# Kernel tuning notes

Measured on AMD Instinct MI355X. Metric: run time of the kernel, lower is better.

## Reference

```python
import jax, jax.numpy as jnp
import numpy as np

B, C, N, K, D = 4, 64, 40960, 16, 128
EPS = 1e-5  # BatchNorm2d default eps


def _bn_relu(x, g, b, m, v):
    # inference BN over channel axis 1, then ReLU (pt_utils.Conv2d default activation)
    scale = g / jnp.sqrt(v + EPS)
    shift = b - m * scale
    return jax.nn.relu(x * scale[None, :, None, None] + shift[None, :, None, None])


def setup_inputs() -> dict:
    key = jax.random.key(0)
    ks = jax.random.split(key, 16)
    feature = jax.random.normal(ks[0], (B, C, N, 1), jnp.float32)
    neigh_idx = jax.random.randint(ks[1], (B, N, K), 0, N)
    w1 = jax.random.normal(ks[2], (C, C), jnp.float32) * 0.05
    w2 = jax.random.normal(ks[3], (D, C), jnp.float32) * 0.05
    w3 = jax.random.normal(ks[4], (D, C), jnp.float32) * 0.05
    def bn(kg, km, kv, n):
        g = 1.0 + 0.1 * jax.random.normal(kg, (n,), jnp.float32)
        b = 0.1 * jax.random.normal(km, (n,), jnp.float32)
        m = 0.1 * jax.random.normal(kv, (n,), jnp.float32)
        v = jax.random.uniform(jax.random.fold_in(kv, 1), (n,), jnp.float32, 0.5, 1.5)
        return g, b, m, v
    g1, b1, m1, v1 = bn(ks[5], ks[6], ks[7], C)
    g2, b2, m2, v2 = bn(ks[8], ks[9], ks[10], D)
    g3, b3, m3, v3 = bn(ks[11], ks[12], ks[13], D)
    return dict(feature=feature, neigh_idx=neigh_idx,
                w1=w1, g1=g1, b1=b1, m1=m1, v1=v1,
                w2=w2, g2=g2, b2=b2, m2=m2, v2=v2,
                w3=w3, g3=g3, b3=b3, m3=m3, v3=v3)


def reference(feature, neigh_idx, w1, g1, b1, m1, v1, w2, g2, b2, m2, v2,
              w3, g3, b3, m3, v3):
    # gather_neighbour: feature [B,C,N,1], neigh_idx [B,N,K] -> [B,C,N,K]
    f = feature[:, :, :, 0]                                   # [B,C,N]
    f_neigh = jax.vmap(lambda fb, ib: fb[:, ib])(f, neigh_idx)  # [B,C,N,K]
    # mlp1: 1x1 conv + BN + ReLU
    h = jnp.einsum('oc,bcnk->bonk', w1, f_neigh)
    h = _bn_relu(h, g1, b1, m1, v1)
    # sum over neighbors
    h = jnp.sum(h, axis=-1, keepdims=True)                    # [B,C,N,1]
    # mlp2
    h = jnp.einsum('oc,bcnk->bonk', w2, h)
    h = _bn_relu(h, g2, b2, m2, v2)
    # mlp3 on original feature (residual branch)
    s = jnp.einsum('oc,bcnk->bonk', w3, feature)
    s = _bn_relu(s, g3, b3, m3, v3)
    return h + s                                              # [B,D,N,1]
```

## Files before the change

kernel.cpp:

```cpp
#include <hip/hip_runtime.h>

#define EPSV 1e-5f
constexpr int Bb = 4, Cc = 64, Nn = 40960, Kk = 16, Dd = 128;
constexpr int G = 5;
constexpr int TPB = Nn / 16;

typedef float f32x4 __attribute__((ext_vector_type(4)));
typedef __bf16 bf16x8 __attribute__((ext_vector_type(8)));
typedef unsigned short us8 __attribute__((ext_vector_type(8)));
typedef unsigned short us4 __attribute__((ext_vector_type(4)));

__device__ inline unsigned short f2bf(float x) {
    unsigned u = __builtin_bit_cast(unsigned, x);
    u += 0x7FFFu + ((u >> 16) & 1u);
    return (unsigned short)(u >> 16);
}

__global__ __launch_bounds__(256) void prep_weights(
    const float* __restrict__ w1, const float* __restrict__ g1, const float* __restrict__ b1,
    const float* __restrict__ m1, const float* __restrict__ v1,
    const float* __restrict__ w2, const float* __restrict__ g2, const float* __restrict__ b2,
    const float* __restrict__ m2, const float* __restrict__ v2,
    const float* __restrict__ w3, const float* __restrict__ g3, const float* __restrict__ b3,
    const float* __restrict__ m3, const float* __restrict__ v3,
    unsigned short* __restrict__ w1s, unsigned short* __restrict__ w2s, unsigned short* __restrict__ w3s,
    float* __restrict__ sh1, float* __restrict__ sh2, float* __restrict__ sh3) {
    const int e = blockIdx.x * 256 + threadIdx.x;
    if (e < 4096) {
        const int o = e >> 6;
        const float sc = g1[o] * rsqrtf(v1[o] + EPSV);
        w1s[e] = f2bf(w1[e] * sc);
    } else if (e < 12288) {
        const int i = e - 4096, o = i >> 6;
        const float sc = g2[o] * rsqrtf(v2[o] + EPSV);
        w2s[i] = f2bf(w2[i] * sc);
    } else if (e < 20480) {
        const int i = e - 12288, o = i >> 6;
        const float sc = g3[o] * rsqrtf(v3[o] + EPSV);
        w3s[i] = f2bf(w3[i] * sc);
    }
    if (e < 64) sh1[e] = b1[e] - m1[e] * (g1[e] * rsqrtf(v1[e] + EPSV));
    else if (e < 192) { const int d = e - 64;  sh2[d] = b2[d] - m2[d] * (g2[d] * rsqrtf(v2[d] + EPSV)); }
    else if (e < 320) { const int d = e - 192; sh3[d] = b3[d] - m3[d] * (g3[d] * rsqrtf(v3[d] + EPSV)); }
}

__global__ __launch_bounds__(256) void passA(const float* __restrict__ f,
                                             const unsigned short* __restrict__ w1s,
                                             unsigned short* __restrict__ G1) {
    __shared__ float s[64 * 65];
    __shared__ __attribute__((aligned(16))) unsigned short sg1[64 * 72];

    const int tid = threadIdx.x, w = tid >> 6, lane = tid & 63;
    const int c15 = lane & 15, q = lane >> 4;
    const int b = blockIdx.x / 640;
    const int n0 = (blockIdx.x % 640) * 64;

    const float* src = f + ((size_t)b * Cc + w * 16) * Nn + n0 + lane;
#pragma unroll
    for (int i = 0; i < 16; ++i) s[(w * 16 + i) * 65 + lane] = src[(size_t)i * Nn];

    const int o1 = w * 16 + c15;
    bf16x8 bw1[2];
#pragma unroll
    for (int ks = 0; ks < 2; ++ks)
        bw1[ks] = __builtin_bit_cast(bf16x8, *(const uint4*)(w1s + o1 * 64 + ks * 32 + q * 8));
    __syncthreads();

#pragma unroll
    for (int mt = 0; mt < 4; ++mt) {
        const int pt = mt * 16 + c15;
        us8 A0, A1;
#pragma unroll
        for (int j = 0; j < 8; ++j) A0[j] = f2bf(s[(q * 8 + j) * 65 + pt]);
#pragma unroll
        for (int j = 0; j < 8; ++j) A1[j] = f2bf(s[(32 + q * 8 + j) * 65 + pt]);
        f32x4 g = {0.f, 0.f, 0.f, 0.f};
        g = __builtin_amdgcn_mfma_f32_16x16x32_bf16(__builtin_bit_cast(bf16x8, A0), bw1[0], g, 0, 0, 0);
        g = __builtin_amdgcn_mfma_f32_16x16x32_bf16(__builtin_bit_cast(bf16x8, A1), bw1[1], g, 0, 0, 0);
#pragma unroll
        for (int r = 0; r < 4; ++r) sg1[(mt * 16 + q * 4 + r) * 72 + o1] = f2bf(g[r]);
    }
    __syncthreads();

    {
        const int p = tid >> 2, ck = tid & 3;
        const uint4 v0 = *(const uint4*)(sg1 + p * 72 + ck * 16);
        const uint4 v1 = *(const uint4*)(sg1 + p * 72 + ck * 16 + 8);
        unsigned short* dst = G1 + ((size_t)b * Nn + n0 + p) * 64 + ck * 16;
        *(uint4*)dst = v0;
        *(uint4*)(dst + 8) = v1;
    }
}

__global__ __launch_bounds__(256, 4) void passB(
    const unsigned short* __restrict__ G1, const float* __restrict__ f,
    const int* __restrict__ idx,
    const unsigned short* __restrict__ w2s, const unsigned short* __restrict__ w3s,
    const float* __restrict__ sh1, const float* __restrict__ sh2, const float* __restrict__ sh3,
    float* __restrict__ out) {
    __shared__ __attribute__((aligned(16))) unsigned short s_h1[16 * 72];
    __shared__ float s_out[16 * 132];

    const int tid  = threadIdx.x;
    const int wave = tid >> 6;
    const int lane = tid & 63;
    const int c15  = lane & 15;
    const int q    = lane >> 4;
    const int pg   = tid >> 4;
    const int cg   = tid & 15;

    const int t0  = blockIdx.x * G;
    const int b   = t0 / TPB;
    const int nb0 = (t0 - b * TPB) * 16;

    float sh2v[2], sh3v[2];
    bf16x8 bw2[2][2], bw3[2][2];
#pragma unroll
    for (int nt = 0; nt < 2; ++nt) {
        const int d = wave * 32 + nt * 16 + c15;
        sh2v[nt] = sh2[d];
        sh3v[nt] = sh3[d];
#pragma unroll
        for (int ks = 0; ks < 2; ++ks) {
            bw2[nt][ks] = __builtin_bit_cast(bf16x8, *(const uint4*)(w2s + d * 64 + ks * 32 + q * 8));
            bw3[nt][ks] = __builtin_bit_cast(bf16x8, *(const uint4*)(w3s + d * 64 + ks * 32 + q * 8));
        }
    }
    float shA[4];
#pragma unroll
    for (int j = 0; j < 4; ++j) shA[j] = sh1[cg * 4 + j];

    const unsigned short* G1b = G1 + (size_t)b * Nn * 64;
    const float* fb0 = f + (size_t)b * Cc * Nn;

    for (int g = 0; g < G; ++g) {
        const int n0 = nb0 + g * 16;

        const float* fown = fb0 + n0 + c15;
        us8 F0, F1;
#pragma unroll
        for (int j = 0; j < 8; ++j) F0[j] = f2bf(fown[(size_t)(q * 8 + j) * Nn]);
#pragma unroll
        for (int j = 0; j < 8; ++j) F1[j] = f2bf(fown[(size_t)(32 + q * 8 + j) * Nn]);

        const int myidx = idx[((size_t)b * Nn + n0) * Kk + tid];

        float a0 = 0.f, a1 = 0.f, a2 = 0.f, a3 = 0.f;
#pragma unroll
        for (int k = 0; k < 16; ++k) {
            const int nb = __shfl(myidx, (pg & 3) * 16 + k, 64);
            const uint2 d2 = *(const uint2*)(G1b + (size_t)nb * 64 + cg * 4);
            const float f0 = __builtin_bit_cast(float, d2.x << 16);
            const float f1 = __builtin_bit_cast(float, d2.x & 0xffff0000u);
            const float f2v = __builtin_bit_cast(float, d2.y << 16);
            const float f3 = __builtin_bit_cast(float, d2.y & 0xffff0000u);
            a0 += fmaxf(f0 + shA[0], 0.f);
            a1 += fmaxf(f1 + shA[1], 0.f);
            a2 += fmaxf(f2v + shA[2], 0.f);
            a3 += fmaxf(f3 + shA[3], 0.f);
        }

        __syncthreads();
        us4 hv;
        hv[0] = f2bf(a0); hv[1] = f2bf(a1); hv[2] = f2bf(a2); hv[3] = f2bf(a3);
        *(us4*)(s_h1 + pg * 72 + cg * 4) = hv;
        __syncthreads();

        const unsigned short* h1row = s_h1 + c15 * 72;
        const bf16x8 ah0 = __builtin_bit_cast(bf16x8, *(const uint4*)(h1row + q * 8));
        const bf16x8 ah1 = __builtin_bit_cast(bf16x8, *(const uint4*)(h1row + 32 + q * 8));
        const bf16x8 af0 = __builtin_bit_cast(bf16x8, F0);
        const bf16x8 af1 = __builtin_bit_cast(bf16x8, F1);

#pragma unroll
        for (int nt = 0; nt < 2; ++nt) {
            f32x4 h2 = {sh2v[nt], sh2v[nt], sh2v[nt], sh2v[nt]};
            f32x4 s3 = {sh3v[nt], sh3v[nt], sh3v[nt], sh3v[nt]};
            h2 = __builtin_amdgcn_mfma_f32_16x16x32_bf16(ah0, bw2[nt][0], h2, 0, 0, 0);
            h2 = __builtin_amdgcn_mfma_f32_16x16x32_bf16(ah1, bw2[nt][1], h2, 0, 0, 0);
            s3 = __builtin_amdgcn_mfma_f32_16x16x32_bf16(af0, bw3[nt][0], s3, 0, 0, 0);
            s3 = __builtin_amdgcn_mfma_f32_16x16x32_bf16(af1, bw3[nt][1], s3, 0, 0, 0);
            const int d = wave * 32 + nt * 16 + c15;
#pragma unroll
            for (int r = 0; r < 4; ++r) {
                const int p = q * 4 + r;
                s_out[p * 132 + d] = fmaxf(h2[r], 0.f) + fmaxf(s3[r], 0.f);
            }
        }
        __syncthreads();

        {
            const int d = tid >> 1, half = tid & 1;
            float v[8];
#pragma unroll
            for (int i = 0; i < 8; ++i) v[i] = s_out[(half * 8 + i) * 132 + d];
            float* dst = out + ((size_t)b * Dd + d) * Nn + n0 + half * 8;
            __builtin_nontemporal_store((f32x4){v[0], v[1], v[2], v[3]}, (f32x4*)dst);
            __builtin_nontemporal_store((f32x4){v[4], v[5], v[6], v[7]}, (f32x4*)(dst + 4));
        }
    }
}

extern "C" void kernel_launch(void* const* d_in, const int* in_sizes, int n_in,
                              void* d_out, int out_size, void* d_ws, size_t ws_size,
                              hipStream_t stream) {
    const float* feature = (const float*)d_in[0];
    const int*   neigh   = (const int*)d_in[1];
    const float* w1 = (const float*)d_in[2];
    const float* g1 = (const float*)d_in[3];
    const float* b1 = (const float*)d_in[4];
    const float* m1 = (const float*)d_in[5];
    const float* v1 = (const float*)d_in[6];
    const float* w2 = (const float*)d_in[7];
    const float* g2 = (const float*)d_in[8];
    const float* b2 = (const float*)d_in[9];
    const float* m2 = (const float*)d_in[10];
    const float* v2 = (const float*)d_in[11];
    const float* w3 = (const float*)d_in[12];
    const float* g3 = (const float*)d_in[13];
    const float* b3 = (const float*)d_in[14];
    const float* m3 = (const float*)d_in[15];
    const float* v3 = (const float*)d_in[16];
    float* out = (float*)d_out;

    char* ws = (char*)d_ws;
    unsigned short* G1  = (unsigned short*)ws;
    unsigned short* w1s = (unsigned short*)(ws + 20971520);
    unsigned short* w2s = (unsigned short*)(ws + 20971520 + 8192);
    unsigned short* w3s = (unsigned short*)(ws + 20971520 + 24576);
    float* sh1 = (float*)(ws + 20971520 + 40960);
    float* sh2 = (float*)(ws + 20971520 + 41216);
    float* sh3 = (float*)(ws + 20971520 + 41728);

    prep_weights<<<80, 256, 0, stream>>>(w1, g1, b1, m1, v1, w2, g2, b2, m2, v2,
                                         w3, g3, b3, m3, v3, w1s, w2s, w3s, sh1, sh2, sh3);
    passA<<<Bb * 640, 256, 0, stream>>>(feature, w1s, G1);
    passB<<<(Bb * TPB) / G, 256, 0, stream>>>(G1, feature, neigh, w2s, w3s,
                                              sh1, sh2, sh3, out);
}
```

Measured before the change: 227.8 us.

## Stage transposed bf16 features in passA and store outputs directly from MFMA

passA now also writes a point-major bf16 copy of the input features, provided the workspace is large enough, so passB loads its residual-branch operand as contiguous 16-byte vectors instead of 16 strided fp32 loads per lane. passB drops the shared-memory output staging and its extra barrier, and each lane writes its four MFMA results straight to global memory as one f32x4. Groups per block rise from 5 to 8. The trade-off is an extra 20 MB write and read of the transposed copy, plus narrower, less coalesced output stores.

```diff
diff --git a/kernel.cpp b/kernel.cpp
--- a/kernel.cpp
+++ b/kernel.cpp
@@ -2,7 +2,7 @@
 
 #define EPSV 1e-5f
 constexpr int Bb = 4, Cc = 64, Nn = 40960, Kk = 16, Dd = 128;
-constexpr int G = 5;
+constexpr int G = 8;
 constexpr int TPB = Nn / 16;
 
 typedef float f32x4 __attribute__((ext_vector_type(4)));
@@ -46,7 +46,9 @@
 
 __global__ __launch_bounds__(256) void passA(const float* __restrict__ f,
                                              const unsigned short* __restrict__ w1s,
-                                             unsigned short* __restrict__ G1) {
+                                             unsigned short* __restrict__ G1,
+                                             unsigned short* __restrict__ ft,
+                                             int use_ft) {
     __shared__ float s[64 * 65];
     __shared__ __attribute__((aligned(16))) unsigned short sg1[64 * 72];
 
@@ -65,6 +67,18 @@
     for (int ks = 0; ks < 2; ++ks)
         bw1[ks] = __builtin_bit_cast(bf16x8, *(const uint4*)(w1s + o1 * 64 + ks * 32 + q * 8));
     __syncthreads();
+
+    if (use_ft) {
+        const int p = tid >> 2, ck = tid & 3;
+        us8 o0, o1v;
+#pragma unroll
+        for (int j = 0; j < 8; ++j) o0[j] = f2bf(s[(ck * 16 + j) * 65 + p]);
+#pragma unroll
+        for (int j = 0; j < 8; ++j) o1v[j] = f2bf(s[(ck * 16 + 8 + j) * 65 + p]);
+        unsigned short* dst = ft + ((size_t)b * Nn + n0 + p) * 64 + ck * 16;
+        *(us8*)dst = o0;
+        *(us8*)(dst + 8) = o1v;
+    }
 
 #pragma unroll
     for (int mt = 0; mt < 4; ++mt) {
@@ -93,13 +107,12 @@
 }
 
 __global__ __launch_bounds__(256, 4) void passB(
-    const unsigned short* __restrict__ G1, const float* __restrict__ f,
-    const int* __restrict__ idx,
+    const unsigned short* __restrict__ G1, const unsigned short* __restrict__ ft,
+    const float* __restrict__ f, const int* __restrict__ idx,
     const unsigned short* __restrict__ w2s, const unsigned short* __restrict__ w3s,
     const float* __restrict__ sh1, const float* __restrict__ sh2, const float* __restrict__ sh3,
-    float* __restrict__ out) {
+    float* __restrict__ out, int use_ft) {
     __shared__ __attribute__((aligned(16))) unsigned short s_h1[16 * 72];
-    __shared__ float s_out[16 * 132];
 
     const int tid  = threadIdx.x;
     const int wave = tid >> 6;
@@ -131,17 +144,24 @@
     for (int j = 0; j < 4; ++j) shA[j] = sh1[cg * 4 + j];
 
     const unsigned short* G1b = G1 + (size_t)b * Nn * 64;
+    const unsigned short* ftb = ft + (size_t)b * Nn * 64;
     const float* fb0 = f + (size_t)b * Cc * Nn;
 
     for (int g = 0; g < G; ++g) {
         const int n0 = nb0 + g * 16;
 
-        const float* fown = fb0 + n0 + c15;
         us8 F0, F1;
-#pragma unroll
-        for (int j = 0; j < 8; ++j) F0[j] = f2bf(fown[(size_t)(q * 8 + j) * Nn]);
-#pragma unroll
-        for (int j = 0; j < 8; ++j) F1[j] = f2bf(fown[(size_t)(32 + q * 8 + j) * Nn]);
+        if (use_ft) {
+            const unsigned short* frow = ftb + (size_t)(n0 + c15) * 64;
+            F0 = *(const us8*)(frow + q * 8);
+            F1 = *(const us8*)(frow + 32 + q * 8);
+        } else {
+            const float* fown = fb0 + n0 + c15;
+#pragma unroll
+            for (int j = 0; j < 8; ++j) F0[j] = f2bf(fown[(size_t)(q * 8 + j) * Nn]);
+#pragma unroll
+            for (int j = 0; j < 8; ++j) F1[j] = f2bf(fown[(size_t)(32 + q * 8 + j) * Nn]);
+        }
 
         const int myidx = idx[((size_t)b * Nn + n0) * Kk + tid];
 
@@ -181,22 +201,10 @@
             s3 = __builtin_amdgcn_mfma_f32_16x16x32_bf16(af0, bw3[nt][0], s3, 0, 0, 0);
             s3 = __builtin_amdgcn_mfma_f32_16x16x32_bf16(af1, bw3[nt][1], s3, 0, 0, 0);
             const int d = wave * 32 + nt * 16 + c15;
-#pragma unroll
-            for (int r = 0; r < 4; ++r) {
-                const int p = q * 4 + r;
-                s_out[p * 132 + d] = fmaxf(h2[r], 0.f) + fmaxf(s3[r], 0.f);
-            }
-        }
-        __syncthreads();
-
-        {
-            const int d = tid >> 1, half = tid & 1;
-            float v[8];
-#pragma unroll
-            for (int i = 0; i < 8; ++i) v[i] = s_out[(half * 8 + i) * 132 + d];
-            float* dst = out + ((size_t)b * Dd + d) * Nn + n0 + half * 8;
-            __builtin_nontemporal_store((f32x4){v[0], v[1], v[2], v[3]}, (f32x4*)dst);
-            __builtin_nontemporal_store((f32x4){v[4], v[5], v[6], v[7]}, (f32x4*)(dst + 4));
+            f32x4 o;
+#pragma unroll
+            for (int r = 0; r < 4; ++r) o[r] = fmaxf(h2[r], 0.f) + fmaxf(s3[r], 0.f);
+            *(f32x4*)(out + ((size_t)b * Dd + d) * Nn + n0 + q * 4) = o;
         }
     }
 }
@@ -223,18 +231,22 @@
     const float* v3 = (const float*)d_in[16];
     float* out = (float*)d_out;
 
+    constexpr size_t SZ = (size_t)Bb * Nn * 64 * 2;
     char* ws = (char*)d_ws;
     unsigned short* G1  = (unsigned short*)ws;
-    unsigned short* w1s = (unsigned short*)(ws + 20971520);
-    unsigned short* w2s = (unsigned short*)(ws + 20971520 + 8192);
-    unsigned short* w3s = (unsigned short*)(ws + 20971520 + 24576);
-    float* sh1 = (float*)(ws + 20971520 + 40960);
-    float* sh2 = (float*)(ws + 20971520 + 41216);
-    float* sh3 = (float*)(ws + 20971520 + 41728);
+    unsigned short* ftp = (unsigned short*)(ws + SZ);
+    const int use_ft = (ws_size >= 2 * SZ + 65536) ? 1 : 0;
+    const size_t woff = use_ft ? 2 * SZ : SZ;
+    unsigned short* w1s = (unsigned short*)(ws + woff);
+    unsigned short* w2s = (unsigned short*)(ws + woff + 8192);
+    unsigned short* w3s = (unsigned short*)(ws + woff + 24576);
+    float* sh1 = (float*)(ws + woff + 40960);
+    float* sh2 = (float*)(ws + woff + 41216);
+    float* sh3 = (float*)(ws + woff + 41728);
 
     prep_weights<<<80, 256, 0, stream>>>(w1, g1, b1, m1, v1, w2, g2, b2, m2, v2,
                                          w3, g3, b3, m3, v3, w1s, w2s, w3s, sh1, sh2, sh3);
-    passA<<<Bb * 640, 256, 0, stream>>>(feature, w1s, G1);
-    passB<<<(Bb * TPB) / G, 256, 0, stream>>>(G1, feature, neigh, w2s, w3s,
-                                              sh1, sh2, sh3, out);
-}
+    passA<<<Bb * 640, 256, 0, stream>>>(feature, w1s, G1, ftp, use_ft);
+    passB<<<(Bb * TPB) / G, 256, 0, stream>>>(G1, ftp, feature, neigh, w2s, w3s,
+                                              sh1, sh2, sh3, out, use_ft);
+}
```

Result: no change. 232.1 us (+1.9%).
